# Kernel tuning notes

Hardware: AMD Instinct MI355X
Metric: run time of the kernel (lower is better)

## Reference

```python
import jax, jax.numpy as jnp
import numpy as np

N, E, IN, HID, H, OUT, G = 50000, 800000, 128, 64, 4, 40, 8
D = HID * H  # 256, concat-head feature dim
NEG_SLOPE = 0.2
EPS = 1e-5


def setup_inputs() -> dict:
    key = jax.random.key(0)
    ks = iter(jax.random.split(key, 40))
    def w(shape, s=0.05):
        return jax.random.normal(next(ks), shape, jnp.float32) * s
    inp = {
        "x": jax.random.normal(next(ks), (N, IN), jnp.float32),
        "edge_index": jax.random.randint(next(ks), (2, E), 0, N),
        "batch": jnp.sort(jax.random.randint(next(ks), (N,), 0, G)),
        # encoder MLP (depth 1): Linear -> LayerNorm -> ReLU -> Linear
        "enc_w1": w((IN, HID)), "enc_b1": jnp.zeros(HID),
        "enc_g": jnp.ones(HID), "enc_be": jnp.zeros(HID),
        "enc_w2": w((HID, HID)), "enc_b2": jnp.zeros(HID),
        # GAT layer 0: in=HID, out=HID, heads=H
        "conv0_w": w((HID, D)), "conv0_as": w((H, HID)), "conv0_ad": w((H, HID)), "conv0_b": jnp.zeros(D),
        # GAT layer 1: in=D, out=HID, heads=H
        "conv1_w": w((D, D)), "conv1_as": w((H, HID)), "conv1_ad": w((H, HID)), "conv1_b": jnp.zeros(D),
        # GAT layer 2 (appended, use_dec=True): in=D, out=HID, heads=H
        "conv2_w": w((D, D)), "conv2_as": w((H, HID)), "conv2_ad": w((H, HID)), "conv2_b": jnp.zeros(D),
        # decoder MLP: Linear -> LayerNorm -> ReLU -> Linear
        "dec_w1": w((D, HID)), "dec_b1": jnp.zeros(HID),
        "dec_g": jnp.ones(HID), "dec_be": jnp.zeros(HID),
        "dec_w2": w((HID, OUT)), "dec_b2": jnp.zeros(OUT),
    }
    return inp


def layernorm(x, g, b):
    m = jnp.mean(x, -1, keepdims=True)
    v = jnp.mean(jnp.square(x - m), -1, keepdims=True)
    return g * (x - m) * jax.lax.rsqrt(v + EPS) + b


def gat_layer(x, src, dst, W, a_src, a_dst, bias):
    # x: [N, F_in]; PyG GATConv with add_self_loops (src/dst already include them)
    h = (x @ W).reshape(N, H, HID)                      # [N, H, C]
    al_s = jnp.einsum('nhc,hc->nh', h, a_src)           # [N, H]
    al_d = jnp.einsum('nhc,hc->nh', h, a_dst)
    e = al_s[src] + al_d[dst]                           # [E', H]
    e = jnp.where(e > 0, e, NEG_SLOPE * e)              # leaky_relu
    m = jax.ops.segment_max(e, dst, num_segments=N)     # per-target softmax
    e = jnp.exp(e - m[dst])
    s = jax.ops.segment_sum(e, dst, num_segments=N)
    alpha = e / (s[dst] + 1e-16)                        # [E', H]
    out = jax.ops.segment_sum(h[src] * alpha[:, :, None], dst, num_segments=N)
    return out.reshape(N, D) + bias                     # concat heads + bias


def reference(x, edge_index, batch,
              enc_w1, enc_b1, enc_g, enc_be, enc_w2, enc_b2,
              conv0_w, conv0_as, conv0_ad, conv0_b,
              conv1_w, conv1_as, conv1_ad, conv1_b,
              conv2_w, conv2_as, conv2_ad, conv2_b,
              dec_w1, dec_b1, dec_g, dec_be, dec_w2, dec_b2):
    loop = jnp.arange(N, dtype=edge_index.dtype)
    src = jnp.concatenate([edge_index[0], loop])
    dst = jnp.concatenate([edge_index[1], loop])
    # encoder MLP
    h = jax.nn.relu(layernorm(x @ enc_w1 + enc_b1, enc_g, enc_be)) @ enc_w2 + enc_b2
    # stacked GAT layers, each followed by ELU
    for (W, a_s, a_d, b) in ((conv0_w, conv0_as, conv0_ad, conv0_b),
                             (conv1_w, conv1_as, conv1_ad, conv1_b),
                             (conv2_w, conv2_as, conv2_ad, conv2_b)):
        h = jax.nn.elu(gat_layer(h, src, dst, W, a_s, a_d, b))
    # global mean pool
    sums = jax.ops.segment_sum(h, batch, num_segments=G)          # [G, D]
    cnt = jax.ops.segment_sum(jnp.ones((N, 1), h.dtype), batch, num_segments=G)
    pooled = sums / jnp.maximum(cnt, 1.0)
    # decoder MLP
    out = jax.nn.relu(layernorm(pooled @ dec_w1 + dec_b1, dec_g, dec_be)) @ dec_w2 + dec_b2
    return out
```

## Files before the change

kernel.cpp:

```cpp
#include <hip/hip_runtime.h>
#include <hip/hip_bf16.h>

#define N_NODES 50000
#define E_EDGES 800000
#define IN_F 128
#define HIDF 64
#define HEADS 4
#define OUT_F 40
#define GROUPS 8
#define D_F 256
#define NEG 0.2f
#define LNEPS 1e-5f
#define POOL_CHUNK 128
#define POOL_BLOCKS ((N_NODES + POOL_CHUNK - 1) / POOL_CHUNK)
#define NB256 ((N_NODES + 255) / 256)

#define OFF_X    0
#define OFF_EW1  6400000
#define OFF_EB1  6408192
#define OFF_EG   6408256
#define OFF_EBE  6408320
#define OFF_EW2  6408384
#define OFF_EB2  6412480
#define OFF_C0W  6412544
#define OFF_C0AS 6428928
#define OFF_C0AD 6429184
#define OFF_C0B  6429440
#define OFF_C1W  6429696
#define OFF_C1AS 6495232
#define OFF_C1AD 6495488
#define OFF_C1B  6495744
#define OFF_C2W  6496000
#define OFF_C2AS 6561536
#define OFF_C2AD 6561792
#define OFF_C2B  6562048
#define OFF_DW1  6562304
#define OFF_DB1  6578688
#define OFF_DG   6578752
#define OFF_DBE  6578816
#define OFF_DW2  6578880
#define OFF_DB2  6581440
#define CANON_TOT 6581480

__device__ __constant__ int c_off[26] = {
    OFF_X, OFF_EW1, OFF_EB1, OFF_EG, OFF_EBE, OFF_EW2, OFF_EB2,
    OFF_C0W, OFF_C0AS, OFF_C0AD, OFF_C0B,
    OFF_C1W, OFF_C1AS, OFF_C1AD, OFF_C1B,
    OFF_C2W, OFF_C2AS, OFF_C2AD, OFF_C2B,
    OFF_DW1, OFF_DB1, OFF_DG, OFF_DBE, OFF_DW2, OFF_DB2, CANON_TOT};

typedef __attribute__((ext_vector_type(8))) short bf16x8;
typedef __attribute__((ext_vector_type(4))) float f32x4;

__device__ __forceinline__ float bf2f(unsigned short u) {
    union { unsigned int i; float f; } v; v.i = ((unsigned int)u) << 16; return v.f;
}
__device__ __forceinline__ unsigned short f2bf(float f) {
    union { float f; unsigned int i; } v; v.f = f;
    unsigned int r = v.i + 0x7FFF + ((v.i >> 16) & 1);
    return (unsigned short)(r >> 16);
}
__device__ __forceinline__ void mac8(float* acc, float w, uint4 u) {
    acc[0] = fmaf(w, bf2f((unsigned short)(u.x & 0xffff)), acc[0]);
    acc[1] = fmaf(w, bf2f((unsigned short)(u.x >> 16)),    acc[1]);
    acc[2] = fmaf(w, bf2f((unsigned short)(u.y & 0xffff)), acc[2]);
    acc[3] = fmaf(w, bf2f((unsigned short)(u.y >> 16)),    acc[3]);
    acc[4] = fmaf(w, bf2f((unsigned short)(u.z & 0xffff)), acc[4]);
    acc[5] = fmaf(w, bf2f((unsigned short)(u.z >> 16)),    acc[5]);
    acc[6] = fmaf(w, bf2f((unsigned short)(u.w & 0xffff)), acc[6]);
    acc[7] = fmaf(w, bf2f((unsigned short)(u.w >> 16)),    acc[7]);
}

__global__ void flag_k(const unsigned short* __restrict__ encg, int* __restrict__ flag) {
    if (threadIdx.x == 0 && blockIdx.x == 0) {
        unsigned short a = encg[0], b = encg[1];
        int f = 0;
        if (a == 0x0000 && b == 0x3F80) f = 1;
        *flag = f;
    }
}

struct SP { const void* q[25]; };
__global__ __launch_bounds__(256) void convert_k(SP sp, const int* __restrict__ flag,
                                                 unsigned short* __restrict__ canon) {
    int i = blockIdx.x * 256 + threadIdx.x;
    if (i >= CANON_TOT) return;
    int fl = *flag;
    if (i < OFF_EW1) {
        canon[i] = fl == 0 ? ((const unsigned short*)sp.q[0])[i]
                           : f2bf(((const float*)sp.q[0])[i]);
        return;
    }
    int t = 1;
    while (i >= c_off[t + 1]) ++t;
    int j = i - c_off[t];
    const void* s = sp.q[t];
    canon[i] = fl == 0 ? ((const unsigned short*)s)[j] : f2bf(((const float*)s)[j]);
}

__global__ void wt_k(const unsigned short* __restrict__ canon,
                     unsigned short* __restrict__ wt0, unsigned short* __restrict__ wt1,
                     unsigned short* __restrict__ wt2, unsigned short* __restrict__ w1t,
                     unsigned short* __restrict__ w2t) {
    int i = blockIdx.x * 256 + threadIdx.x;
    if (i < 8192) {
        int k = i >> 6, n = i & 63;
        w1t[n * 128 + k] = canon[OFF_EW1 + k * 64 + n];
    }
    if (i < 4096) {
        int k = i >> 6, n = i & 63;
        w2t[n * 64 + k] = canon[OFF_EW2 + k * 64 + n];
    }
    if (i < 16384) {
        int k = i >> 8, n = i & 255;
        wt0[n * 64 + k] = canon[OFF_C0W + i];
    }
    if (i < 65536) {
        int k = i >> 8, n = i & 255;
        wt1[n * 256 + k] = canon[OFF_C1W + i];
        wt2[n * 256 + k] = canon[OFF_C2W + i];
    }
}

__global__ __launch_bounds__(128) void enc1_k(const unsigned short* __restrict__ canon,
                                              const unsigned short* __restrict__ w1t,
                                              unsigned short* __restrict__ T1) {
    const unsigned short* x = canon + OFF_X;
    __shared__ unsigned short As[128 * 72];
    __shared__ unsigned short Bs[64 * 72];
    int tid = threadIdx.x, wave = tid >> 6, lane = tid & 63;
    int q = lane >> 4, l = lane & 15;
    int row0 = blockIdx.x * 128;
    f32x4 acc[4][4];
#pragma unroll
    for (int a = 0; a < 4; ++a)
#pragma unroll
        for (int b = 0; b < 4; ++b) acc[a][b] = (f32x4){0.f, 0.f, 0.f, 0.f};
    for (int kb = 0; kb < IN_F; kb += 64) {
#pragma unroll
        for (int it = 0; it < 8; ++it) {
            int cid = it * 128 + tid;
            int r = cid >> 3, kc = cid & 7;
            int gr = row0 + r;
            uint4 v = make_uint4(0, 0, 0, 0);
            if (gr < N_NODES) v = *(const uint4*)(x + (size_t)gr * IN_F + kb + kc * 8);
            *(uint4*)&As[r * 72 + kc * 8] = v;
        }
#pragma unroll
        for (int it = 0; it < 4; ++it) {
            int cid = it * 128 + tid;
            int r = cid >> 3, kc = cid & 7;
            uint4 w = *(const uint4*)(w1t + (size_t)r * IN_F + kb + kc * 8);
            *(uint4*)&Bs[r * 72 + kc * 8] = w;
        }
        __syncthreads();
#pragma unroll
        for (int ks = 0; ks < 64; ks += 32) {
            bf16x8 af[4], bfr[4];
#pragma unroll
            for (int mt = 0; mt < 4; ++mt)
                af[mt] = *(const bf16x8*)&As[(wave * 64 + mt * 16 + l) * 72 + ks + q * 8];
#pragma unroll
            for (int nt = 0; nt < 4; ++nt)
                bfr[nt] = *(const bf16x8*)&Bs[(nt * 16 + l) * 72 + ks + q * 8];
#pragma unroll
            for (int mt = 0; mt < 4; ++mt)
#pragma unroll
                for (int nt = 0; nt < 4; ++nt)
                    acc[mt][nt] = __builtin_amdgcn_mfma_f32_16x16x32_bf16(
                        af[mt], bfr[nt], acc[mt][nt], 0, 0, 0);
        }
        __syncthreads();
    }
    float b1c[4], gc[4], bec[4];
#pragma unroll
    for (int nt = 0; nt < 4; ++nt) {
        int c = nt * 16 + l;
        b1c[nt] = bf2f(canon[OFF_EB1 + c]);
        gc[nt]  = bf2f(canon[OFF_EG + c]);
        bec[nt] = bf2f(canon[OFF_EBE + c]);
    }
#pragma unroll
    for (int mt = 0; mt < 4; ++mt) {
#pragma unroll
        for (int r = 0; r < 4; ++r) {
            int grow = row0 + wave * 64 + mt * 16 + q * 4 + r;
            float v0 = acc[mt][0][r] + b1c[0];
            float v1 = acc[mt][1][r] + b1c[1];
            float v2 = acc[mt][2][r] + b1c[2];
            float v3 = acc[mt][3][r] + b1c[3];
            float s = v0 + v1 + v2 + v3;
#pragma unroll
            for (int off = 1; off < 16; off <<= 1) s += __shfl_xor(s, off);
            float mean = s * (1.0f / 64.0f);
            float d0 = v0 - mean, d1 = v1 - mean, d2 = v2 - mean, d3 = v3 - mean;
            float vs = d0 * d0 + d1 * d1 + d2 * d2 + d3 * d3;
#pragma unroll
            for (int off = 1; off < 16; off <<= 1) vs += __shfl_xor(vs, off);
            float rstd = rsqrtf(vs * (1.0f / 64.0f) + LNEPS);
            if (grow < N_NODES) {
                unsigned short* trow = T1 + (size_t)grow * HIDF;
                float o0 = gc[0] * d0 * rstd + bec[0]; o0 = fmaxf(o0, 0.f);
                float o1 = gc[1] * d1 * rstd + bec[1]; o1 = fmaxf(o1, 0.f);
                float o2 = gc[2] * d2 * rstd + bec[2]; o2 = fmaxf(o2, 0.f);
                float o3 = gc[3] * d3 * rstd + bec[3]; o3 = fmaxf(o3, 0.f);
                trow[l] = f2bf(o0); trow[16 + l] = f2bf(o1);
                trow[32 + l] = f2bf(o2); trow[48 + l] = f2bf(o3);
            }
        }
    }
}

__global__ __launch_bounds__(128) void enc2_k(const unsigned short* __restrict__ canon,
                                              const unsigned short* __restrict__ T1,
                                              const unsigned short* __restrict__ w2t,
                                              unsigned short* __restrict__ h0) {
    __shared__ unsigned short As[128 * 72];
    __shared__ unsigned short Bs[64 * 72];
    int tid = threadIdx.x, wave = tid >> 6, lane = tid & 63;
    int q = lane >> 4, l = lane & 15;
    int row0 = blockIdx.x * 128;
    f32x4 acc[4][4];
#pragma unroll
    for (int a = 0; a < 4; ++a)
#pragma unroll
        for (int b = 0; b < 4; ++b) acc[a][b] = (f32x4){0.f, 0.f, 0.f, 0.f};
#pragma unroll
    for (int it = 0; it < 8; ++it) {
        int cid = it * 128 + tid;
        int r = cid >> 3, kc = cid & 7;
        int gr = row0 + r;
        uint4 v = make_uint4(0, 0, 0, 0);
        if (gr < N_NODES) v = *(const uint4*)(T1 + (size_t)gr * HIDF + kc * 8);
        *(uint4*)&As[r * 72 + kc * 8] = v;
    }
#pragma unroll
    for (int it = 0; it < 4; ++it) {
        int cid = it * 128 + tid;
        int r = cid >> 3, kc = cid & 7;
        uint4 w = *(const uint4*)(w2t + (size_t)r * HIDF + kc * 8);
        *(uint4*)&Bs[r * 72 + kc * 8] = w;
    }
    __syncthreads();
#pragma unroll
    for (int ks = 0; ks < 64; ks += 32) {
        bf16x8 af[4], bfr[4];
#pragma unroll
        for (int mt = 0; mt < 4; ++mt)
            af[mt] = *(const bf16x8*)&As[(wave * 64 + mt * 16 + l) * 72 + ks + q * 8];
#pragma unroll
        for (int nt = 0; nt < 4; ++nt)
            bfr[nt] = *(const bf16x8*)&Bs[(nt * 16 + l) * 72 + ks + q * 8];
#pragma unroll
        for (int mt = 0; mt < 4; ++mt)
#pragma unroll
            for (int nt = 0; nt < 4; ++nt)
                acc[mt][nt] = __builtin_amdgcn_mfma_f32_16x16x32_bf16(
                    af[mt], bfr[nt], acc[mt][nt], 0, 0, 0);
    }
    float b2c[4];
#pragma unroll
    for (int nt = 0; nt < 4; ++nt) b2c[nt] = bf2f(canon[OFF_EB2 + nt * 16 + l]);
#pragma unroll
    for (int mt = 0; mt < 4; ++mt) {
#pragma unroll
        for (int r = 0; r < 4; ++r) {
            int grow = row0 + wave * 64 + mt * 16 + q * 4 + r;
            if (grow < N_NODES) {
                unsigned short* hrow = h0 + (size_t)grow * HIDF;
#pragma unroll
                for (int nt = 0; nt < 4; ++nt)
                    hrow[nt * 16 + l] = f2bf(acc[mt][nt][r] + b2c[nt]);
            }
        }
    }
}

__global__ void deg_init_k(int* __restrict__ deg) {
    int i = blockIdx.x * 256 + threadIdx.x;
    if (i < N_NODES) deg[i] = 1;
}
__global__ void deg_count_k(const int* __restrict__ dstI, int* __restrict__ deg) {
    int i = blockIdx.x * 256 + threadIdx.x;
    if (i < E_EDGES) atomicAdd(&deg[dstI[i]], 1);
}
__global__ __launch_bounds__(256) void scan1_k(const int* __restrict__ deg, int* __restrict__ excl,
                                               int* __restrict__ bsums) {
    int tid = threadIdx.x, lane = tid & 63, wv = tid >> 6;
    int gid = blockIdx.x * 256 + tid;
    int v = (gid < N_NODES) ? deg[gid] : 0;
    int inc = v;
#pragma unroll
    for (int off = 1; off < 64; off <<= 1) { int t = __shfl_up(inc, off); if (lane >= off) inc += t; }
    __shared__ int wsum[4];
    if (lane == 63) wsum[wv] = inc;
    __syncthreads();
    int wo = 0;
    for (int w = 0; w < wv; ++w) wo += wsum[w];
    int incl = inc + wo;
    if (gid < N_NODES) excl[gid] = incl - v;
    if (tid == 255) bsums[blockIdx.x] = incl;
}
__global__ __launch_bounds__(256) void scan2_k(const int* __restrict__ bsums, int* __restrict__ boff,
                                               int* __restrict__ totalp) {
    int tid = threadIdx.x, lane = tid & 63, wv = tid >> 6;
    int v = (tid < NB256) ? bsums[tid] : 0;
    int inc = v;
#pragma unroll
    for (int off = 1; off < 64; off <<= 1) { int t = __shfl_up(inc, off); if (lane >= off) inc += t; }
    __shared__ int wsum[4];
    if (lane == 63) wsum[wv] = inc;
    __syncthreads();
    int wo = 0;
    for (int w = 0; w < wv; ++w) wo += wsum[w];
    int incl = inc + wo;
    if (tid < NB256) boff[tid] = incl - v;
    if (tid == 255) *totalp = incl;
}
__global__ void scan3_k(const int* __restrict__ excl, const int* __restrict__ boff,
                        int* __restrict__ rowp, int* __restrict__ cursor) {
    int i = blockIdx.x * 256 + threadIdx.x;
    if (i < N_NODES) { int r = excl[i] + boff[i >> 8]; rowp[i] = r; cursor[i] = r; }
}
__global__ void fill_k(const int* __restrict__ srcI, const int* __restrict__ dstI,
                       int* __restrict__ cursor, int* __restrict__ colx) {
    int i = blockIdx.x * 256 + threadIdx.x;
    if (i >= E_EDGES + N_NODES) return;
    int s, d;
    if (i < E_EDGES) { s = srcI[i]; d = dstI[i]; } else { s = i - E_EDGES; d = s; }
    int slot = atomicAdd(&cursor[d], 1);
    colx[slot] = s;
}

__global__ __launch_bounds__(256) void mfma_mm_k(
    const unsigned short* __restrict__ A, const unsigned short* __restrict__ Wt,
    unsigned short* __restrict__ C, int M, int K,
    const unsigned short* __restrict__ aSv, const unsigned short* __restrict__ aDv,
    float* __restrict__ alS, float* __restrict__ alD) {
    __shared__ unsigned short smem[128 * 72 * 2];
    unsigned short* As = smem;
    unsigned short* Bs = smem + 128 * 72;
    int tid = threadIdx.x;
    int wave = tid >> 6, lane = tid & 63;
    int wm = wave >> 1, wn = wave & 1;
    int row0 = blockIdx.y * 128, col0 = blockIdx.x * 128;
    int q = lane >> 4, l = lane & 15;
    f32x4 acc[4][4];
#pragma unroll
    for (int a = 0; a < 4; ++a)
#pragma unroll
        for (int b = 0; b < 4; ++b) acc[a][b] = (f32x4){0.f, 0.f, 0.f, 0.f};
    for (int kb = 0; kb < K; kb += 64) {
#pragma unroll
        for (int it = 0; it < 4; ++it) {
            int cid = it * 256 + tid;
            int r = cid >> 3, kc = cid & 7;
            int gr = row0 + r;
            uint4 v = make_uint4(0, 0, 0, 0);
            if (gr < M) v = *(const uint4*)(A + (size_t)gr * K + kb + kc * 8);
            *(uint4*)&As[r * 72 + kc * 8] = v;
            int gn = col0 + r;
            uint4 w = *(const uint4*)(Wt + (size_t)gn * K + kb + kc * 8);
            *(uint4*)&Bs[r * 72 + kc * 8] = w;
        }
        __syncthreads();
#pragma unroll
        for (int ks = 0; ks < 64; ks += 32) {
            bf16x8 af[4], bfr[4];
#pragma unroll
            for (int mt = 0; mt < 4; ++mt)
                af[mt] = *(const bf16x8*)&As[(wm * 64 + mt * 16 + l) * 72 + ks + q * 8];
#pragma unroll
            for (int nt = 0; nt < 4; ++nt)
                bfr[nt] = *(const bf16x8*)&Bs[(wn * 64 + nt * 16 + l) * 72 + ks + q * 8];
#pragma unroll
            for (int mt = 0; mt < 4; ++mt)
#pragma unroll
                for (int nt = 0; nt < 4; ++nt)
                    acc[mt][nt] = __builtin_amdgcn_mfma_f32_16x16x32_bf16(
                        af[mt], bfr[nt], acc[mt][nt], 0, 0, 0);
        }
        __syncthreads();
    }
#pragma unroll
    for (int mt = 0; mt < 4; ++mt) {
        int rowb = wm * 64 + mt * 16 + q * 4;
#pragma unroll
        for (int r = 0; r < 4; ++r) {
#pragma unroll
            for (int nt = 0; nt < 4; ++nt)
                smem[(rowb + r) * 136 + wn * 64 + nt * 16 + l] = f2bf(acc[mt][nt][r]);
        }
    }
    __syncthreads();
    int row = tid >> 1, half = tid & 1;
    int grow = row0 + row;
    if (grow < M) {
        unsigned short* crow = C + (size_t)grow * D_F + col0 + half * 64;
        const unsigned short* srow = &smem[row * 136 + half * 64];
#pragma unroll
        for (int i = 0; i < 8; ++i)
            *(uint4*)(crow + i * 8) = *(const uint4*)(srow + i * 8);
        int head = (col0 >> 6) + half;
        const unsigned short* av = aSv + head * 64;
        const unsigned short* dv = aDv + head * 64;
        float ps = 0.f, pd = 0.f;
#pragma unroll
        for (int k = 0; k < 64; ++k) {
            float hv = bf2f(srow[k]);
            ps = fmaf(hv, bf2f(av[k]), ps);
            pd = fmaf(hv, bf2f(dv[k]), pd);
        }
        alS[(size_t)grow * 4 + head] = ps;
        alD[(size_t)grow * 4 + head] = pd;
    }
}

__global__ __launch_bounds__(256) void aggpre_k(
    const int* __restrict__ rowp, const int* __restrict__ colx,
    const float* __restrict__ alS, const float* __restrict__ alD,
    unsigned short* __restrict__ alphaBuf, float* __restrict__ rinvBuf) {
    int tid = threadIdx.x, wave = tid >> 6, lane = tid & 63;
    int n = blockIdx.x * 4 + wave;
    if (n >= N_NODES) return;
    int start = rowp[n], end = rowp[n + 1];
    float4 ad = *(const float4*)(alD + (size_t)n * 4);
    float l0 = 0.f, l1 = 0.f, l2 = 0.f, l3 = 0.f;
    for (int j = start + lane; j < end; j += 64) {
        int s = colx[j];
        float4 as = *(const float4*)(alS + (size_t)s * 4);
        float e0 = as.x + ad.x; e0 = e0 > 0.f ? e0 : NEG * e0;
        float e1 = as.y + ad.y; e1 = e1 > 0.f ? e1 : NEG * e1;
        float e2 = as.z + ad.z; e2 = e2 > 0.f ? e2 : NEG * e2;
        float e3 = as.w + ad.w; e3 = e3 > 0.f ? e3 : NEG * e3;
        ushort4 a;
        a.x = f2bf(__expf(e0)); a.y = f2bf(__expf(e1));
        a.z = f2bf(__expf(e2)); a.w = f2bf(__expf(e3));
        *(ushort4*)(alphaBuf + (size_t)j * 4) = a;
        l0 += bf2f(a.x); l1 += bf2f(a.y); l2 += bf2f(a.z); l3 += bf2f(a.w);
    }
#pragma unroll
    for (int off = 1; off < 64; off <<= 1) {
        l0 += __shfl_xor(l0, off); l1 += __shfl_xor(l1, off);
        l2 += __shfl_xor(l2, off); l3 += __shfl_xor(l3, off);
    }
    if (lane == 0) {
        *(float4*)(rinvBuf + (size_t)n * 4) = make_float4(
            1.f / (l0 + 1e-16f), 1.f / (l1 + 1e-16f),
            1.f / (l2 + 1e-16f), 1.f / (l3 + 1e-16f));
    }
}

__global__ __launch_bounds__(256) void agg2_k(
    const unsigned short* __restrict__ h2, const int* __restrict__ rowp, const int* __restrict__ colx,
    const unsigned short* __restrict__ alphaBuf, const float* __restrict__ rinvBuf,
    const unsigned short* __restrict__ bias, unsigned short* __restrict__ out) {
    int tid = threadIdx.x, wave = tid >> 6, lane = tid & 63;
    int n = blockIdx.x * 4 + wave;
    if (n >= N_NODES) return;
    int start = rowp[n], end = rowp[n + 1];
    int e = lane >> 5;
    int c = lane & 31;
    int head = c >> 3;
    float acc[8] = {};
    int j = start;
    for (; j + 3 < end; j += 4) {
        int j1 = j + e, j2 = j + 2 + e;
        int s1 = colx[j1], s2 = colx[j2];
        float w1 = bf2f(alphaBuf[(size_t)j1 * 4 + head]);
        float w2 = bf2f(alphaBuf[(size_t)j2 * 4 + head]);
        uint4 u1 = *(const uint4*)(h2 + (size_t)s1 * D_F + c * 8);
        uint4 u2 = *(const uint4*)(h2 + (size_t)s2 * D_F + c * 8);
        mac8(acc, w1, u1);
        mac8(acc, w2, u2);
    }
    for (; j < end; j += 2) {
        int j1 = j + e;
        int jc = j1 < end ? j1 : end - 1;
        int s1 = colx[jc];
        float w1 = (j1 < end) ? bf2f(alphaBuf[(size_t)jc * 4 + head]) : 0.f;
        uint4 u1 = *(const uint4*)(h2 + (size_t)s1 * D_F + c * 8);
        mac8(acc, w1, u1);
    }
#pragma unroll
    for (int k = 0; k < 8; ++k) acc[k] += __shfl_xor(acc[k], 32);
    if (lane < 32) {
        float rh = rinvBuf[(size_t)n * 4 + head];
        uint4 bu = *(const uint4*)(bias + c * 8);
        float b[8];
        b[0] = bf2f((unsigned short)(bu.x & 0xffff)); b[1] = bf2f((unsigned short)(bu.x >> 16));
        b[2] = bf2f((unsigned short)(bu.y & 0xffff)); b[3] = bf2f((unsigned short)(bu.y >> 16));
        b[4] = bf2f((unsigned short)(bu.z & 0xffff)); b[5] = bf2f((unsigned short)(bu.z >> 16));
        b[6] = bf2f((unsigned short)(bu.w & 0xffff)); b[7] = bf2f((unsigned short)(bu.w >> 16));
        unsigned int o[4];
#pragma unroll
        for (int k = 0; k < 4; ++k) {
            float v0 = acc[2 * k] * rh + b[2 * k];
            float v1 = acc[2 * k + 1] * rh + b[2 * k + 1];
            v0 = v0 > 0.f ? v0 : __expf(v0) - 1.f;
            v1 = v1 > 0.f ? v1 : __expf(v1) - 1.f;
            o[k] = (unsigned int)f2bf(v0) | ((unsigned int)f2bf(v1) << 16);
        }
        *(uint4*)(out + (size_t)n * D_F + c * 8) = make_uint4(o[0], o[1], o[2], o[3]);
    }
}

__global__ __launch_bounds__(256) void pool_k(const unsigned short* __restrict__ h,
                                              const int* __restrict__ batch,
                                              float* __restrict__ part, int* __restrict__ pcnt) {
    __shared__ float sums[GROUPS * D_F];
    __shared__ int cnts[GROUPS];
    int tid = threadIdx.x;
    for (int i = tid; i < GROUPS * D_F; i += 256) sums[i] = 0.f;
    if (tid < GROUPS) cnts[tid] = 0;
    __syncthreads();
    int n0 = blockIdx.x * POOL_CHUNK;
    int n1 = n0 + POOL_CHUNK; if (n1 > N_NODES) n1 = N_NODES;
    for (int n = n0; n < n1; ++n) {
        int b = batch[n];
        sums[b * D_F + tid] += bf2f(h[(size_t)n * D_F + tid]);
        if (tid == 0) cnts[b]++;
    }
    __syncthreads();
    float* po = part + (size_t)blockIdx.x * (GROUPS * D_F);
    for (int i = tid; i < GROUPS * D_F; i += 256) po[i] = sums[i];
    if (tid < GROUPS) pcnt[blockIdx.x * GROUPS + tid] = cnts[tid];
}

__global__ __launch_bounds__(256) void reduce_k(const float* __restrict__ part,
                                                const int* __restrict__ pcnt,
                                                float* __restrict__ gsum, int* __restrict__ gcnt) {
    int g = blockIdx.x, c = threadIdx.x;
    float s = 0.f;
    for (int b = 0; b < POOL_BLOCKS; ++b) s += part[(size_t)b * (GROUPS * D_F) + g * D_F + c];
    gsum[g * D_F + c] = s;
    if (threadIdx.x < 64) {
        int lane = threadIdx.x;
        int cn = 0;
        for (int b = lane; b < POOL_BLOCKS; b += 64) cn += pcnt[b * GROUPS + g];
#pragma unroll
        for (int off = 1; off < 64; off <<= 1) cn += __shfl_xor(cn, off);
        if (lane == 0) gcnt[g] = cn;
    }
}

__global__ __launch_bounds__(256) void dec_k(const float* __restrict__ gsum, const int* __restrict__ gcnt,
    const unsigned short* __restrict__ canon, const int* __restrict__ flag,
    void* __restrict__ outp) {
    const unsigned short* w1 = canon + OFF_DW1;
    const unsigned short* b1 = canon + OFF_DB1;
    const unsigned short* gam = canon + OFF_DG;
    const unsigned short* bet = canon + OFF_DBE;
    const unsigned short* w2 = canon + OFF_DW2;
    const unsigned short* b2 = canon + OFF_DB2;
    int tid = threadIdx.x, grp = blockIdx.x * 4 + (tid >> 6), lane = tid & 63;
    if (grp >= GROUPS) return;
    float inv = 1.0f / fmaxf((float)gcnt[grp], 1.0f);
    float p[4];
#pragma unroll
    for (int i = 0; i < 4; ++i) p[i] = gsum[grp * D_F + i * 64 + lane] * inv;
    float acc = bf2f(b1[lane]);
#pragma unroll
    for (int i = 0; i < 4; ++i)
        for (int k = 0; k < 64; ++k)
            acc = fmaf(__shfl(p[i], k), bf2f(w1[(i * 64 + k) * 64 + lane]), acc);
    float s = acc;
#pragma unroll
    for (int off = 32; off > 0; off >>= 1) s += __shfl_xor(s, off);
    float mean = s * (1.0f / 64.0f);
    float d = acc - mean;
    float vs = d * d;
#pragma unroll
    for (int off = 32; off > 0; off >>= 1) vs += __shfl_xor(vs, off);
    float rstd = rsqrtf(vs * (1.0f / 64.0f) + LNEPS);
    float val = bf2f(gam[lane]) * d * rstd + bf2f(bet[lane]);
    val = val > 0.f ? val : val * 0.f;
    int cl = (lane < OUT_F) ? lane : 0;
    float acc2 = 0.f;
    for (int k = 0; k < 64; ++k) {
        float wv = bf2f(w2[k * OUT_F + cl]);
        acc2 = fmaf(__shfl(val, k), wv, acc2);
    }
    if (lane < OUT_F) {
        float res = acc2 + bf2f(b2[lane]);
        if (*flag == 0) ((unsigned short*)outp)[grp * OUT_F + lane] = f2bf(res);
        else            ((float*)outp)[grp * OUT_F + lane] = res;
    }
}

extern "C" void kernel_launch(void* const* d_in, const int* in_sizes, int n_in,
                              void* d_out, int out_size, void* d_ws, size_t ws_size,
                              hipStream_t stream) {
    const int* ei    = (const int*)d_in[1];
    const int* batch = (const int*)d_in[2];

    char* p = (char*)d_ws;
    unsigned short* canon = (unsigned short*)p; p += (size_t)CANON_TOT * 2 + 16;
    unsigned short* bufA = (unsigned short*)p; p += (size_t)N_NODES * D_F * 2;
    unsigned short* bufB = (unsigned short*)p; p += (size_t)N_NODES * D_F * 2;
    unsigned short* wt0 = (unsigned short*)p; p += (size_t)64 * 256 * 2;
    unsigned short* wt1 = (unsigned short*)p; p += (size_t)256 * 256 * 2;
    unsigned short* wt2 = (unsigned short*)p; p += (size_t)256 * 256 * 2;
    unsigned short* w1t = (unsigned short*)p; p += (size_t)64 * 128 * 2;
    unsigned short* w2t = (unsigned short*)p; p += (size_t)64 * 64 * 2;
    float* alS  = (float*)p; p += (size_t)N_NODES * 4 * 4;
    float* alD  = (float*)p; p += (size_t)N_NODES * 4 * 4;
    float* rinvB = (float*)p; p += (size_t)N_NODES * 4 * 4;
    unsigned short* alphaB = (unsigned short*)p; p += (size_t)(E_EDGES + N_NODES) * 4 * 2;
    float* part = (float*)p; p += (size_t)POOL_BLOCKS * GROUPS * D_F * 4;
    int* pcnt   = (int*)p;   p += (size_t)POOL_BLOCKS * GROUPS * 4;
    float* gsum = (float*)p; p += GROUPS * D_F * 4;
    int* gcnt   = (int*)p;   p += 16 * 4;
    int* deg    = (int*)p;   p += (size_t)N_NODES * 4;
    int* excl   = (int*)p;   p += (size_t)N_NODES * 4;
    int* bsums  = (int*)p;   p += 256 * 4;
    int* boff   = (int*)p;   p += 256 * 4;
    int* rowp   = (int*)p;   p += (size_t)(N_NODES + 4) * 4;
    int* cursor = (int*)p;   p += (size_t)N_NODES * 4;
    int* colx   = (int*)p;   p += (size_t)(E_EDGES + N_NODES) * 4;
    int* flag   = (int*)p;   p += 16;

    const int* srcI = ei;
    const int* dstI = ei + E_EDGES;

    SP sp;
    sp.q[0] = d_in[0];
    for (int t = 1; t < 25; ++t) sp.q[t] = d_in[t + 2];

    int nwb = (N_NODES + 3) / 4;
    int nb128 = (N_NODES + 127) / 128;

    flag_k<<<1, 64, 0, stream>>>((const unsigned short*)d_in[5], flag);
    convert_k<<<(CANON_TOT + 255) / 256, 256, 0, stream>>>(sp, flag, canon);
    wt_k<<<256, 256, 0, stream>>>(canon, wt0, wt1, wt2, w1t, w2t);

    enc1_k<<<nb128, 128, 0, stream>>>(canon, w1t, bufB);
    enc2_k<<<nb128, 128, 0, stream>>>(canon, bufB, w2t, bufA);

    deg_init_k<<<NB256, 256, 0, stream>>>(deg);
    deg_count_k<<<(E_EDGES + 255) / 256, 256, 0, stream>>>(dstI, deg);
    scan1_k<<<NB256, 256, 0, stream>>>(deg, excl, bsums);
    scan2_k<<<1, 256, 0, stream>>>(bsums, boff, rowp + N_NODES);
    scan3_k<<<NB256, 256, 0, stream>>>(excl, boff, rowp, cursor);
    fill_k<<<(E_EDGES + N_NODES + 255) / 256, 256, 0, stream>>>(srcI, dstI, cursor, colx);

    dim3 mmg(2, nb128);
    mfma_mm_k<<<mmg, 256, 0, stream>>>(bufA, wt0, bufB, N_NODES, HIDF,
                                       canon + OFF_C0AS, canon + OFF_C0AD, alS, alD);
    aggpre_k<<<nwb, 256, 0, stream>>>(rowp, colx, alS, alD, alphaB, rinvB);
    agg2_k<<<nwb, 256, 0, stream>>>(bufB, rowp, colx, alphaB, rinvB, canon + OFF_C0B, bufA);

    mfma_mm_k<<<mmg, 256, 0, stream>>>(bufA, wt1, bufB, N_NODES, D_F,
                                       canon + OFF_C1AS, canon + OFF_C1AD, alS, alD);
    aggpre_k<<<nwb, 256, 0, stream>>>(rowp, colx, alS, alD, alphaB, rinvB);
    agg2_k<<<nwb, 256, 0, stream>>>(bufB, rowp, colx, alphaB, rinvB, canon + OFF_C1B, bufA);

    mfma_mm_k<<<mmg, 256, 0, stream>>>(bufA, wt2, bufB, N_NODES, D_F,
                                       canon + OFF_C2AS, canon + OFF_C2AD, alS, alD);
    aggpre_k<<<nwb, 256, 0, stream>>>(rowp, colx, alS, alD, alphaB, rinvB);
    agg2_k<<<nwb, 256, 0, stream>>>(bufB, rowp, colx, alphaB, rinvB, canon + OFF_C2B, bufA);

    pool_k<<<POOL_BLOCKS, 256, 0, stream>>>(bufA, batch, part, pcnt);
    reduce_k<<<GROUPS, 256, 0, stream>>>(part, pcnt, gsum, gcnt);
    dec_k<<<2, 256, 0, stream>>>(gsum, gcnt, canon, flag, d_out);
}
```

Baseline: 661.5 us.

## Fuse attention-weight computation into the GAT aggregation kernel

Removes the separate aggpre kernel that computed exp attention weights and per-node inverse sums into global buffers. The aggregation kernel now recomputes leaky-relu and exp per edge and head inline from alS/alD and accumulates the softmax denominator itself. The main loop is also unrolled from 4 to 8 edges per iteration to expose more memory-level parallelism. This drops three kernel launches and the alpha buffer write/read traffic, at the cost of redundant exp work (each of 8 lanes per head recomputes the same weight) and more register pressure. Weights stay in fp32 instead of being rounded to bf16.

```diff
diff --git a/kernel.cpp b/kernel.cpp
--- a/kernel.cpp
+++ b/kernel.cpp
@@ -416,44 +416,9 @@
     }
 }
 
-__global__ __launch_bounds__(256) void aggpre_k(
-    const int* __restrict__ rowp, const int* __restrict__ colx,
+__global__ __launch_bounds__(256) void agg_k(
+    const unsigned short* __restrict__ h2, const int* __restrict__ rowp, const int* __restrict__ colx,
     const float* __restrict__ alS, const float* __restrict__ alD,
-    unsigned short* __restrict__ alphaBuf, float* __restrict__ rinvBuf) {
-    int tid = threadIdx.x, wave = tid >> 6, lane = tid & 63;
-    int n = blockIdx.x * 4 + wave;
-    if (n >= N_NODES) return;
-    int start = rowp[n], end = rowp[n + 1];
-    float4 ad = *(const float4*)(alD + (size_t)n * 4);
-    float l0 = 0.f, l1 = 0.f, l2 = 0.f, l3 = 0.f;
-    for (int j = start + lane; j < end; j += 64) {
-        int s = colx[j];
-        float4 as = *(const float4*)(alS + (size_t)s * 4);
-        float e0 = as.x + ad.x; e0 = e0 > 0.f ? e0 : NEG * e0;
-        float e1 = as.y + ad.y; e1 = e1 > 0.f ? e1 : NEG * e1;
-        float e2 = as.z + ad.z; e2 = e2 > 0.f ? e2 : NEG * e2;
-        float e3 = as.w + ad.w; e3 = e3 > 0.f ? e3 : NEG * e3;
-        ushort4 a;
-        a.x = f2bf(__expf(e0)); a.y = f2bf(__expf(e1));
-        a.z = f2bf(__expf(e2)); a.w = f2bf(__expf(e3));
-        *(ushort4*)(alphaBuf + (size_t)j * 4) = a;
-        l0 += bf2f(a.x); l1 += bf2f(a.y); l2 += bf2f(a.z); l3 += bf2f(a.w);
-    }
-#pragma unroll
-    for (int off = 1; off < 64; off <<= 1) {
-        l0 += __shfl_xor(l0, off); l1 += __shfl_xor(l1, off);
-        l2 += __shfl_xor(l2, off); l3 += __shfl_xor(l3, off);
-    }
-    if (lane == 0) {
-        *(float4*)(rinvBuf + (size_t)n * 4) = make_float4(
-            1.f / (l0 + 1e-16f), 1.f / (l1 + 1e-16f),
-            1.f / (l2 + 1e-16f), 1.f / (l3 + 1e-16f));
-    }
-}
-
-__global__ __launch_bounds__(256) void agg2_k(
-    const unsigned short* __restrict__ h2, const int* __restrict__ rowp, const int* __restrict__ colx,
-    const unsigned short* __restrict__ alphaBuf, const float* __restrict__ rinvBuf,
     const unsigned short* __restrict__ bias, unsigned short* __restrict__ out) {
     int tid = threadIdx.x, wave = tid >> 6, lane = tid & 63;
     int n = blockIdx.x * 4 + wave;
@@ -462,30 +427,47 @@
     int e = lane >> 5;
     int c = lane & 31;
     int head = c >> 3;
+    float adh = alD[(size_t)n * 4 + head];
     float acc[8] = {};
+    float asum = 0.f;
     int j = start;
-    for (; j + 3 < end; j += 4) {
-        int j1 = j + e, j2 = j + 2 + e;
-        int s1 = colx[j1], s2 = colx[j2];
-        float w1 = bf2f(alphaBuf[(size_t)j1 * 4 + head]);
-        float w2 = bf2f(alphaBuf[(size_t)j2 * 4 + head]);
-        uint4 u1 = *(const uint4*)(h2 + (size_t)s1 * D_F + c * 8);
-        uint4 u2 = *(const uint4*)(h2 + (size_t)s2 * D_F + c * 8);
-        mac8(acc, w1, u1);
-        mac8(acc, w2, u2);
+    for (; j + 7 < end; j += 8) {
+        int ja = j + e, jb = j + 2 + e, jc2 = j + 4 + e, jd = j + 6 + e;
+        int sa = colx[ja], sb = colx[jb], sc = colx[jc2], sd = colx[jd];
+        float ea = alS[(size_t)sa * 4 + head] + adh; ea = ea > 0.f ? ea : NEG * ea;
+        float eb = alS[(size_t)sb * 4 + head] + adh; eb = eb > 0.f ? eb : NEG * eb;
+        float ec = alS[(size_t)sc * 4 + head] + adh; ec = ec > 0.f ? ec : NEG * ec;
+        float ed = alS[(size_t)sd * 4 + head] + adh; ed = ed > 0.f ? ed : NEG * ed;
+        float wa = __expf(ea), wb = __expf(eb), wc = __expf(ec), wd = __expf(ed);
+        uint4 ua = *(const uint4*)(h2 + (size_t)sa * D_F + c * 8);
+        uint4 ub = *(const uint4*)(h2 + (size_t)sb * D_F + c * 8);
+        uint4 uc = *(const uint4*)(h2 + (size_t)sc * D_F + c * 8);
+        uint4 ud = *(const uint4*)(h2 + (size_t)sd * D_F + c * 8);
+        asum += (wa + wb) + (wc + wd);
+        mac8(acc, wa, ua);
+        mac8(acc, wb, ub);
+        mac8(acc, wc, uc);
+        mac8(acc, wd, ud);
     }
     for (; j < end; j += 2) {
         int j1 = j + e;
         int jc = j1 < end ? j1 : end - 1;
         int s1 = colx[jc];
-        float w1 = (j1 < end) ? bf2f(alphaBuf[(size_t)jc * 4 + head]) : 0.f;
+        float w1 = 0.f;
+        if (j1 < end) {
+            float ev = alS[(size_t)s1 * 4 + head] + adh;
+            ev = ev > 0.f ? ev : NEG * ev;
+            w1 = __expf(ev);
+        }
         uint4 u1 = *(const uint4*)(h2 + (size_t)s1 * D_F + c * 8);
+        asum += w1;
         mac8(acc, w1, u1);
     }
 #pragma unroll
     for (int k = 0; k < 8; ++k) acc[k] += __shfl_xor(acc[k], 32);
+    asum += __shfl_xor(asum, 32);
     if (lane < 32) {
-        float rh = rinvBuf[(size_t)n * 4 + head];
+        float rh = 1.f / (asum + 1e-16f);
         uint4 bu = *(const uint4*)(bias + c * 8);
         float b[8];
         b[0] = bf2f((unsigned short)(bu.x & 0xffff)); b[1] = bf2f((unsigned short)(bu.x >> 16));
@@ -605,8 +587,6 @@
     unsigned short* w2t = (unsigned short*)p; p += (size_t)64 * 64 * 2;
     float* alS  = (float*)p; p += (size_t)N_NODES * 4 * 4;
     float* alD  = (float*)p; p += (size_t)N_NODES * 4 * 4;
-    float* rinvB = (float*)p; p += (size_t)N_NODES * 4 * 4;
-    unsigned short* alphaB = (unsigned short*)p; p += (size_t)(E_EDGES + N_NODES) * 4 * 2;
     float* part = (float*)p; p += (size_t)POOL_BLOCKS * GROUPS * D_F * 4;
     int* pcnt   = (int*)p;   p += (size_t)POOL_BLOCKS * GROUPS * 4;
     float* gsum = (float*)p; p += GROUPS * D_F * 4;
@@ -647,18 +627,15 @@
     dim3 mmg(2, nb128);
     mfma_mm_k<<<mmg, 256, 0, stream>>>(bufA, wt0, bufB, N_NODES, HIDF,
                                        canon + OFF_C0AS, canon + OFF_C0AD, alS, alD);
-    aggpre_k<<<nwb, 256, 0, stream>>>(rowp, colx, alS, alD, alphaB, rinvB);
-    agg2_k<<<nwb, 256, 0, stream>>>(bufB, rowp, colx, alphaB, rinvB, canon + OFF_C0B, bufA);
+    agg_k<<<nwb, 256, 0, stream>>>(bufB, rowp, colx, alS, alD, canon + OFF_C0B, bufA);
 
     mfma_mm_k<<<mmg, 256, 0, stream>>>(bufA, wt1, bufB, N_NODES, D_F,
                                        canon + OFF_C1AS, canon + OFF_C1AD, alS, alD);
-    aggpre_k<<<nwb, 256, 0, stream>>>(rowp, colx, alS, alD, alphaB, rinvB);
-    agg2_k<<<nwb, 256, 0, stream>>>(bufB, rowp, colx, alphaB, rinvB, canon + OFF_C1B, bufA);
+    agg_k<<<nwb, 256, 0, stream>>>(bufB, rowp, colx, alS, alD, canon + OFF_C1B, bufA);
 
     mfma_mm_k<<<mmg, 256, 0, stream>>>(bufA, wt2, bufB, N_NODES, D_F,
                                        canon + OFF_C2AS, canon + OFF_C2AD, alS, alD);
-    aggpre_k<<<nwb, 256, 0, stream>>>(rowp, colx, alS, alD, alphaB, rinvB);
-    agg2_k<<<nwb, 256, 0, stream>>>(bufB, rowp, colx, alphaB, rinvB, canon + OFF_C2B, bufA);
+    agg_k<<<nwb, 256, 0, stream>>>(bufB, rowp, colx, alS, alD, canon + OFF_C2B, bufA);
 
     pool_k<<<POOL_BLOCKS, 256, 0, stream>>>(bufA, batch, part, pcnt);
     reduce_k<<<GROUPS, 256, 0, stream>>>(part, pcnt, gsum, gcnt);
```

Measured after the change: 632.0 us. -4.5%, faster.
